# Kernel optimization log

Hardware: AMD Instinct MI355X
Metric: run time of the kernel (lower is better)

Reference implementation:

```python
import jax, jax.numpy as jnp
import numpy as np

N_NODES = 100000
N_EDGES = 1600000
D_FEAT = 32


def setup_inputs() -> dict:
    key = jax.random.key(0)
    k1, k2, k3, k4, k5 = jax.random.split(key, 5)
    src_feats = jax.random.normal(k1, (N_NODES, D_FEAT), dtype=jnp.float32)
    cj = jax.random.uniform(k2, (N_NODES, 1), dtype=jnp.float32)
    ci = jax.random.uniform(k3, (N_NODES, 1), dtype=jnp.float32)
    src_idx = jax.random.randint(k4, (N_EDGES,), 0, N_NODES, dtype=jnp.int32)
    dst_idx = jax.random.randint(k5, (N_EDGES,), 0, N_NODES, dtype=jnp.int32)
    return {"src_feats": src_feats, "cj": cj, "ci": ci,
            "src_idx": src_idx, "dst_idx": dst_idx}


def reference(src_feats, cj, ci, src_idx, dst_idx):
    # Dropout in eval mode (identity). Training-mode dropout is stochastic and
    # excluded from the correctness baseline.
    weighted = src_feats * cj                      # [N, d] scale by src norm coeff
    msgs = weighted[src_idx]                       # [E, d] gather (copy_u)
    agg = jax.ops.segment_sum(msgs, dst_idx, num_segments=N_NODES)  # [N, d] sum aggregate
    return agg * ci                                # [N, d] scale by dst norm coeff
```

## Files before the change

kernel.cpp:

```cpp
#include <hip/hip_runtime.h>
#include <hip/hip_fp16.h>

#define N_NODES 100000
#define N_EDGES 1600000
#define D_FEAT 32
#define CAP 32
#define NPASS 4
#define NODES_PER_P (N_NODES / NPASS)
#define EDGE_THREADS (N_EDGES / 4)
#define EDGE_BLOCKS ((EDGE_THREADS + 255) / 256)

typedef int   __attribute__((ext_vector_type(4))) i32x4;
typedef float __attribute__((ext_vector_type(4))) f32x4;

__global__ __launch_bounds__(256) void lgc_weight(
    const f32x4* __restrict__ feats4,
    const float* __restrict__ cj,
    __half2*     __restrict__ w2)
{
    int tid = blockIdx.x * 256 + threadIdx.x;
    float c = cj[tid >> 3];
    f32x4 v = __builtin_nontemporal_load(&feats4[tid]);
    w2[tid * 2 + 0] = __floats2half2_rn(v.x * c, v.y * c);
    w2[tid * 2 + 1] = __floats2half2_rn(v.z * c, v.w * c);
}

__device__ __forceinline__ void spill_row(const __half* __restrict__ weighted,
                                          float* __restrict__ out, int s, int d)
{
    const __half* row = weighted + (size_t)s * D_FEAT;
    float* o = out + (size_t)d * D_FEAT;
    for (int f = 0; f < D_FEAT; ++f) atomicAdd(o + f, __half2float(row[f]));
}

__global__ __launch_bounds__(256) void lgc_bucket(
    const i32x4*  __restrict__ dst4,
    const i32x4*  __restrict__ src4,
    const __half* __restrict__ weighted,
    int*          __restrict__ cnt,
    int*          __restrict__ bucket,
    float*        __restrict__ out)
{
    int x  = blockIdx.x % NPASS;
    int lb = blockIdx.x / NPASS;
    int t  = lb * 256 + threadIdx.x;
    if (t >= EDGE_THREADS) return;

    const int lo = x * NODES_PER_P;
    const int hi = lo + NODES_PER_P;

    i32x4 d4 = __builtin_nontemporal_load(&dst4[t]);
    bool ix = (d4.x >= lo) & (d4.x < hi);
    bool iy = (d4.y >= lo) & (d4.y < hi);
    bool iz = (d4.z >= lo) & (d4.z < hi);
    bool iw = (d4.w >= lo) & (d4.w < hi);
    if (!(ix | iy | iz | iw)) return;

    i32x4 s4 = __builtin_nontemporal_load(&src4[t]);
    int ds[4] = {d4.x, d4.y, d4.z, d4.w};
    int ss[4] = {s4.x, s4.y, s4.z, s4.w};
    bool in[4] = {ix, iy, iz, iw};

    #pragma unroll
    for (int k = 0; k < 4; ++k) {
        if (!in[k]) continue;
        int d = ds[k], s = ss[k];
        int pos = atomicAdd(&cnt[d], 1);
        if (pos < CAP) {
            bucket[(size_t)d * CAP + pos] = s;
        } else {
            spill_row(weighted, out, s, d);
        }
    }
}

__global__ __launch_bounds__(256) void lgc_gather(
    const uint4* __restrict__ w4,
    const float* __restrict__ ci,
    const int*   __restrict__ cnt,
    const i32x4* __restrict__ bucket4,
    f32x4*       __restrict__ out4)
{
    int tid = blockIdx.x * 256 + threadIdx.x;
    if (tid >= N_NODES * 4) return;
    int n = tid >> 2;
    int q = tid & 3;

    int c = cnt[n];
    if (c > CAP) c = CAP;
    const i32x4* b4 = bucket4 + (size_t)n * (CAP / 4);

    i32x4 r[8];
    #pragma unroll
    for (int j = 0; j < 8; ++j)
        if (j * 4 < c) r[j] = __builtin_nontemporal_load(&b4[j]);

    float acc[8] = {0.f, 0.f, 0.f, 0.f, 0.f, 0.f, 0.f, 0.f};

    #pragma unroll
    for (int b = 0; b < 4; ++b) {
        const int base = b * 8;
        if (base < c) {
            int m = c - base;
            uint4 v[8];
            #pragma unroll
            for (int t = 0; t < 8; ++t) {
                if (t < m) {
                    int s = ((const int*)r)[base + t];
                    v[t] = w4[(size_t)s * 4 + q];
                }
            }
            #pragma unroll
            for (int t = 0; t < 8; ++t) {
                if (t < m) {
                    unsigned ux = v[t].x, uy = v[t].y, uz = v[t].z, uw = v[t].w;
                    float2 f0 = __half22float2(*(__half2*)&ux);
                    float2 f1 = __half22float2(*(__half2*)&uy);
                    float2 f2 = __half22float2(*(__half2*)&uz);
                    float2 f3 = __half22float2(*(__half2*)&uw);
                    acc[0] += f0.x; acc[1] += f0.y; acc[2] += f1.x; acc[3] += f1.y;
                    acc[4] += f2.x; acc[5] += f2.y; acc[6] += f3.x; acc[7] += f3.y;
                }
            }
        }
    }

    float sc = ci[n];
    size_t ob = (size_t)n * 8 + q * 2;
    f32x4 o0 = __builtin_nontemporal_load(&out4[ob]);
    f32x4 o1 = __builtin_nontemporal_load(&out4[ob + 1]);
    f32x4 a0 = {acc[0], acc[1], acc[2], acc[3]};
    f32x4 a1 = {acc[4], acc[5], acc[6], acc[7]};
    __builtin_nontemporal_store((a0 + o0) * sc, &out4[ob]);
    __builtin_nontemporal_store((a1 + o1) * sc, &out4[ob + 1]);
}

__global__ __launch_bounds__(256) void lgc_scatter(
    const float4* __restrict__ src_feats4,
    const float*  __restrict__ cj,
    const int*    __restrict__ src_idx,
    const int*    __restrict__ dst_idx,
    float*        __restrict__ out)
{
    long tid = (long)blockIdx.x * blockDim.x + threadIdx.x;
    const long total = (long)N_EDGES * 8;
    if (tid >= total) return;
    int e  = (int)(tid >> 3);
    int f4 = (int)(tid & 7);
    int s = src_idx[e];
    int d = dst_idx[e];
    float c = cj[s];
    float4 v = src_feats4[s * 8 + f4];
    float* o = out + (size_t)d * D_FEAT + f4 * 4;
    atomicAdd(o + 0, v.x * c);
    atomicAdd(o + 1, v.y * c);
    atomicAdd(o + 2, v.z * c);
    atomicAdd(o + 3, v.w * c);
}

__global__ __launch_bounds__(256) void lgc_scale(
    float4*       __restrict__ out4,
    const float*  __restrict__ ci)
{
    int tid = blockIdx.x * blockDim.x + threadIdx.x;
    const int total = N_NODES * 8;
    if (tid >= total) return;
    float c = ci[tid >> 3];
    float4 v = out4[tid];
    v.x *= c; v.y *= c; v.z *= c; v.w *= c;
    out4[tid] = v;
}

extern "C" void kernel_launch(void* const* d_in, const int* in_sizes, int n_in,
                              void* d_out, int out_size, void* d_ws, size_t ws_size,
                              hipStream_t stream) {
    const float* src_feats = (const float*)d_in[0];
    const float* cj        = (const float*)d_in[1];
    const float* ci        = (const float*)d_in[2];
    const int*   src_idx   = (const int*)d_in[3];
    const int*   dst_idx   = (const int*)d_in[4];
    float*       out       = (float*)d_out;

    const size_t cnt_ints    = 102400;
    const size_t bucket_ints = (size_t)N_NODES * CAP;
    const size_t wfeat_bytes = (size_t)N_NODES * D_FEAT * sizeof(__half);
    const size_t need = (cnt_ints + bucket_ints) * 4 + wfeat_bytes;

    if (ws_size >= need) {
        int*    cnt      = (int*)d_ws;
        int*    bucket   = cnt + cnt_ints;
        __half* weighted = (__half*)(bucket + bucket_ints);

        hipMemsetAsync(cnt, 0, N_NODES * sizeof(int), stream);
        hipMemsetAsync(out, 0, (size_t)out_size * sizeof(float), stream);

        lgc_weight<<<(N_NODES * 8) / 256, 256, 0, stream>>>(
            (const f32x4*)src_feats, cj, (__half2*)weighted);

        lgc_bucket<<<NPASS * EDGE_BLOCKS, 256, 0, stream>>>(
            (const i32x4*)dst_idx, (const i32x4*)src_idx, weighted,
            cnt, bucket, out);

        lgc_gather<<<(N_NODES * 4 + 255) / 256, 256, 0, stream>>>(
            (const uint4*)weighted, ci, cnt, (const i32x4*)bucket, (f32x4*)out);
    } else {
        hipMemsetAsync(out, 0, (size_t)out_size * sizeof(float), stream);
        {
            const long total = (long)N_EDGES * 8;
            const int grid = (int)((total + 255) / 256);
            lgc_scatter<<<grid, 256, 0, stream>>>((const float4*)src_feats, cj,
                                                  src_idx, dst_idx, out);
        }
        {
            const int grid = (N_NODES * 8 + 255) / 256;
            lgc_scale<<<grid, 256, 0, stream>>>((float4*)out, ci);
        }
    }
}
```

Before: 180.3 us.

## Inline bucket counters into rows, fuse zero-init into weight kernel, use 8 passes

Each node's bucket row now holds its counter in slot 0 and up to 31 source indices, so the atomic counter and its entries share a cache line. The gather reads the count and entries together in one row load. The two memsets are removed by zeroing the output and the counters inside the weight kernel. The bucket pass count rises from 4 to 8, which narrows the destination range per pass at the cost of reading the dst indices more times. Rows always load all 8 vectors, and the lower capacity per row may send slightly more edges to the atomic spill path.

```diff
diff --git a/kernel.cpp b/kernel.cpp
--- a/kernel.cpp
+++ b/kernel.cpp
@@ -4,8 +4,8 @@
 #define N_NODES 100000
 #define N_EDGES 1600000
 #define D_FEAT 32
-#define CAP 32
-#define NPASS 4
+#define CAP 31
+#define NPASS 8
 #define NODES_PER_P (N_NODES / NPASS)
 #define EDGE_THREADS (N_EDGES / 4)
 #define EDGE_BLOCKS ((EDGE_THREADS + 255) / 256)
@@ -16,13 +16,18 @@
 __global__ __launch_bounds__(256) void lgc_weight(
     const f32x4* __restrict__ feats4,
     const float* __restrict__ cj,
-    __half2*     __restrict__ w2)
+    __half2*     __restrict__ w2,
+    int*         __restrict__ brow,
+    f32x4*       __restrict__ out4)
 {
     int tid = blockIdx.x * 256 + threadIdx.x;
     float c = cj[tid >> 3];
     f32x4 v = __builtin_nontemporal_load(&feats4[tid]);
     w2[tid * 2 + 0] = __floats2half2_rn(v.x * c, v.y * c);
     w2[tid * 2 + 1] = __floats2half2_rn(v.z * c, v.w * c);
+    f32x4 z = (f32x4)(0.f);
+    __builtin_nontemporal_store(z, &out4[tid]);
+    if (tid < N_NODES) brow[(size_t)tid * 32] = 0;
 }
 
 __device__ __forceinline__ void spill_row(const __half* __restrict__ weighted,
@@ -37,8 +42,7 @@
     const i32x4*  __restrict__ dst4,
     const i32x4*  __restrict__ src4,
     const __half* __restrict__ weighted,
-    int*          __restrict__ cnt,
-    int*          __restrict__ bucket,
+    int*          __restrict__ brow,
     float*        __restrict__ out)
 {
     int x  = blockIdx.x % NPASS;
@@ -65,9 +69,10 @@
     for (int k = 0; k < 4; ++k) {
         if (!in[k]) continue;
         int d = ds[k], s = ss[k];
-        int pos = atomicAdd(&cnt[d], 1);
+        int* row = brow + (size_t)d * 32;
+        int pos = atomicAdd(row, 1);
         if (pos < CAP) {
-            bucket[(size_t)d * CAP + pos] = s;
+            row[1 + pos] = s;
         } else {
             spill_row(weighted, out, s, d);
         }
@@ -77,8 +82,7 @@
 __global__ __launch_bounds__(256) void lgc_gather(
     const uint4* __restrict__ w4,
     const float* __restrict__ ci,
-    const int*   __restrict__ cnt,
-    const i32x4* __restrict__ bucket4,
+    const i32x4* __restrict__ brow4,
     f32x4*       __restrict__ out4)
 {
     int tid = blockIdx.x * 256 + threadIdx.x;
@@ -86,14 +90,15 @@
     int n = tid >> 2;
     int q = tid & 3;
 
-    int c = cnt[n];
-    if (c > CAP) c = CAP;
-    const i32x4* b4 = bucket4 + (size_t)n * (CAP / 4);
-
+    const i32x4* b4 = brow4 + (size_t)n * 8;
     i32x4 r[8];
     #pragma unroll
     for (int j = 0; j < 8; ++j)
-        if (j * 4 < c) r[j] = __builtin_nontemporal_load(&b4[j]);
+        r[j] = __builtin_nontemporal_load(&b4[j]);
+
+    int c = ((const int*)r)[0];
+    if (c > CAP) c = CAP;
+    const int* ent = ((const int*)r) + 1;
 
     float acc[8] = {0.f, 0.f, 0.f, 0.f, 0.f, 0.f, 0.f, 0.f};
 
@@ -106,7 +111,7 @@
             #pragma unroll
             for (int t = 0; t < 8; ++t) {
                 if (t < m) {
-                    int s = ((const int*)r)[base + t];
+                    int s = ent[base + t];
                     v[t] = w4[(size_t)s * 4 + q];
                 }
             }
@@ -181,28 +186,24 @@
     const int*   dst_idx   = (const int*)d_in[4];
     float*       out       = (float*)d_out;
 
-    const size_t cnt_ints    = 102400;
-    const size_t bucket_ints = (size_t)N_NODES * CAP;
+    const size_t brow_ints   = (size_t)N_NODES * 32;
     const size_t wfeat_bytes = (size_t)N_NODES * D_FEAT * sizeof(__half);
-    const size_t need = (cnt_ints + bucket_ints) * 4 + wfeat_bytes;
+    const size_t need = brow_ints * 4 + wfeat_bytes;
 
     if (ws_size >= need) {
-        int*    cnt      = (int*)d_ws;
-        int*    bucket   = cnt + cnt_ints;
-        __half* weighted = (__half*)(bucket + bucket_ints);
-
-        hipMemsetAsync(cnt, 0, N_NODES * sizeof(int), stream);
-        hipMemsetAsync(out, 0, (size_t)out_size * sizeof(float), stream);
+        int*    brow     = (int*)d_ws;
+        __half* weighted = (__half*)(brow + brow_ints);
 
         lgc_weight<<<(N_NODES * 8) / 256, 256, 0, stream>>>(
-            (const f32x4*)src_feats, cj, (__half2*)weighted);
+            (const f32x4*)src_feats, cj, (__half2*)weighted, brow,
+            (f32x4*)out);
 
         lgc_bucket<<<NPASS * EDGE_BLOCKS, 256, 0, stream>>>(
             (const i32x4*)dst_idx, (const i32x4*)src_idx, weighted,
-            cnt, bucket, out);
+            brow, out);
 
         lgc_gather<<<(N_NODES * 4 + 255) / 256, 256, 0, stream>>>(
-            (const uint4*)weighted, ci, cnt, (const i32x4*)bucket, (f32x4*)out);
+            (const uint4*)weighted, ci, (const i32x4*)brow, (f32x4*)out);
     } else {
         hipMemsetAsync(out, 0, (size_t)out_size * sizeof(float), stream);
         {
```

New measurement: 303.8 us. 68.5% more time.
